# Kernel tuning notes

Measured on AMD Instinct MI355X. Metric: run time of the kernel, lower is better.

The kernel has to match this reference:

```python
import jax, jax.numpy as jnp
import numpy as np

B, N, D, C, K = 16, 1024, 64, 64, 20
EPS = 1e-3  # keras BatchNormalization default epsilon


def _bn(x, g, b, mu, v):
    return (x - mu) * jax.lax.rsqrt(v + EPS) * g + b


def setup_inputs() -> dict:
    key = jax.random.key(0)
    ks = jax.random.split(key, 6)
    return {
        "feats": jax.random.normal(ks[0], (B, N, D), dtype=jnp.float32),
        "adj": jax.random.uniform(ks[1], (B, N, N), dtype=jnp.float32),
        "w1": jax.random.normal(ks[2], (2 * D, C), dtype=jnp.float32) * 0.05,
        "b1": jax.random.normal(ks[3], (C,), dtype=jnp.float32) * 0.05,
        "g1": jnp.ones((C,), jnp.float32),
        "be1": jnp.zeros((C,), jnp.float32),
        "mu1": jnp.zeros((C,), jnp.float32),
        "v1": jnp.ones((C,), jnp.float32),
        "w2": jax.random.normal(ks[4], (C, C), dtype=jnp.float32) * 0.05,
        "b2": jax.random.normal(ks[5], (C,), dtype=jnp.float32) * 0.05,
        "g2": jnp.ones((C,), jnp.float32),
        "be2": jnp.zeros((C,), jnp.float32),
        "mu2": jnp.zeros((C,), jnp.float32),
        "v2": jnp.ones((C,), jnp.float32),
        "k": K,
    }


def reference(feats, adj, w1, b1, g1, be1, mu1, v1, w2, b2, g2, be2, mu2, v2, k):
    # weighted distance matrix from feature channel 0
    f0 = feats[:, :, 0]                                   # (B,N)
    fdiff = jnp.abs(f0[:, None, :] - f0[:, :, None])       # |f[j]-f[i]| at (b,i,j)
    a = adj * fdiff                                        # (B,N,N)
    # KNN: top_k of negated distance
    _, nn_idx = jax.lax.top_k(-a, k)                       # (B,N,k)
    # edge feature gather
    knn_fts = jax.vmap(lambda f, idx: f[idx])(feats, nn_idx)          # (B,N,k,D)
    center = jnp.broadcast_to(feats[:, :, None, :], knn_fts.shape)    # (B,N,k,D)
    edge = jnp.concatenate([center, knn_fts - center], axis=-1)       # (B,N,k,2D)
    # two fused 1x1 conv + BN + ReLU
    x = jax.nn.relu(_bn(jnp.einsum('bnkd,dc->bnkc', edge, w1) + b1, g1, be1, mu1, v1))
    x = jax.nn.relu(_bn(jnp.einsum('bnkc,ce->bnke', x, w2) + b2, g2, be2, mu2, v2))
    # mean over neighbors
    return jnp.mean(x, axis=2)                             # (B,N,C)
```

## Files before the change

kernel.cpp:

```cpp
#include <hip/hip_runtime.h>
#include <float.h>
#include <math.h>

#define NN 1024
#define DD 64
#define CC 64
#define KK 20
#define EPSL 1e-3f

typedef __attribute__((ext_vector_type(8))) short short8;
typedef __attribute__((ext_vector_type(4))) float f32x4;

__device__ __forceinline__ unsigned short f2bf(float f) {
    unsigned u = __float_as_uint(f);
    return (unsigned short)((u + 0x7fffu + ((u >> 16) & 1u)) >> 16);
}

__global__ __launch_bounds__(256) void k0_f0(const float* __restrict__ feats,
                                             float* __restrict__ f0c) {
    int u = blockIdx.x * 256 + threadIdx.x;
    f0c[u] = feats[(size_t)u * DD];
}

__global__ __launch_bounds__(256) void k2_topk_prep(
        const float* __restrict__ adj, const float* __restrict__ f0c,
        const float* __restrict__ w1, const float* __restrict__ w2,
        const float* __restrict__ b1, const float* __restrict__ g1,
        const float* __restrict__ be1, const float* __restrict__ mu1,
        const float* __restrict__ v1,
        unsigned short* __restrict__ b1t, unsigned short* __restrict__ w2t,
        float* __restrict__ bb, int* __restrict__ nnidx) {
    int t = blockIdx.x * 256 + threadIdx.x;
    if (t < 8192) {
        int n = t >> 6, k = t & 63;
        float val;
        if (n < 64) {
            float s = g1[n] * rsqrtf(v1[n] + EPSL);
            val = (w1[k * CC + n] - w1[(k + DD) * CC + n]) * s;
        } else {
            int c = n - 64;
            float s = g1[c] * rsqrtf(v1[c] + EPSL);
            val = w1[(k + DD) * CC + c] * s;
        }
        b1t[t] = f2bf(val);
    } else if (t < 12288) {
        int i = t - 8192;
        int n = i >> 6, k = i & 63;
        w2t[i] = f2bf(w2[k * CC + n]);
    } else if (t < 12352) {
        int c = t - 12288;
        float s = g1[c] * rsqrtf(v1[c] + EPSL);
        bb[c] = b1[c] * s + be1[c] - mu1[c] * s;
    }

    int lane = threadIdx.x & 63;
    int w    = threadIdx.x >> 6;
    int row  = blockIdx.x * 4 + w;
    int b    = row >> 10;
    __shared__ unsigned long long keybuf[4][64];
    const float4* arow = (const float4*)(adj + (size_t)row * NN);
    const float4* frow = (const float4*)(f0c + (size_t)b * NN);
    float f0i = f0c[row];
    unsigned vu[16];
#pragma unroll
    for (int tv = 0; tv < 4; ++tv) {
        float4 av = arow[64 * tv + lane];
        float4 fv = frow[64 * tv + lane];
        vu[tv * 4 + 0] = __float_as_uint(av.x * fabsf(fv.x - f0i));
        vu[tv * 4 + 1] = __float_as_uint(av.y * fabsf(fv.y - f0i));
        vu[tv * 4 + 2] = __float_as_uint(av.z * fabsf(fv.z - f0i));
        vu[tv * 4 + 3] = __float_as_uint(av.w * fabsf(fv.w - f0i));
    }
    unsigned x = vu[0];
#pragma unroll
    for (int tt = 1; tt < 16; ++tt) x = (vu[tt] < x) ? vu[tt] : x;
#pragma unroll
    for (int k = 2; k <= 64; k <<= 1) {
#pragma unroll
        for (int j = k >> 1; j > 0; j >>= 1) {
            unsigned o = __shfl_xor(x, j);
            bool keepmin = (((lane & j) == 0) == ((lane & k) == 0));
            unsigned mn = (o < x) ? o : x;
            unsigned mx = (o < x) ? x : o;
            x = keepmin ? mn : mx;
        }
    }
    unsigned T = __shfl(x, 19);
    int cnt = 0;
#pragma unroll
    for (int tt = 0; tt < 16; ++tt) cnt += (vu[tt] <= T) ? 1 : 0;
    int inc = cnt;
#pragma unroll
    for (int off = 1; off < 64; off <<= 1) {
        int o = __shfl_up(inc, off);
        if (lane >= off) inc += o;
    }
    int total = __shfl(inc, 63);
    int* outp = nnidx + (size_t)row * KK;

    if (total <= 64) {
        int pos = inc - cnt;
#pragma unroll
        for (int tt = 0; tt < 16; ++tt) {
            if (vu[tt] <= T) {
                int j = 256 * (tt >> 2) + 4 * lane + (tt & 3);
                keybuf[w][pos] = ((unsigned long long)vu[tt] << 32) | (unsigned)j;
                pos++;
            }
        }
        unsigned long long key = (lane < total) ? keybuf[w][lane] : ~0ull;
        unsigned y = (unsigned)(key >> 32);
#pragma unroll
        for (int k = 2; k <= 64; k <<= 1) {
#pragma unroll
            for (int j = k >> 1; j > 0; j >>= 1) {
                unsigned o = __shfl_xor(y, j);
                bool keepmin = (((lane & j) == 0) == ((lane & k) == 0));
                unsigned mn = (o < y) ? o : y;
                unsigned mx = (o < y) ? y : o;
                y = keepmin ? mn : mx;
            }
        }
        unsigned Tstar = __shfl(y, 19);
        bool fl = (lane < total) && ((unsigned)(key >> 32) <= Tstar);
        unsigned long long msk = __ballot(fl);
        int p = __popcll(msk & ((1ull << lane) - 1ull));
        if (fl && p < KK) outp[p] = (int)(unsigned)key;
    } else {
        for (int r = 0; r < KK; ++r) {
            unsigned bv = vu[0];
            int bt = 0;
#pragma unroll
            for (int tt = 1; tt < 16; ++tt) {
                if (vu[tt] < bv) { bv = vu[tt]; bt = tt; }
            }
            int bj = 256 * (bt >> 2) + 4 * lane + (bt & 3);
            unsigned wv = bv;
            int wi = bj;
#pragma unroll
            for (int m = 1; m < 64; m <<= 1) {
                unsigned ov = __shfl_xor(wv, m);
                int oi = __shfl_xor(wi, m);
                if (ov < wv || (ov == wv && oi < wi)) { wv = ov; wi = oi; }
            }
            if (lane == 0) outp[r] = wi;
            if (((wi >> 2) & 63) == lane) {
                int s = ((wi >> 8) << 2) | (wi & 3);
#pragma unroll
                for (int tt = 0; tt < 16; ++tt) {
                    if (tt == s) vu[tt] = 0xFFFFFFFFu;
                }
            }
        }
    }
}

__global__ __launch_bounds__(256) void k1_mfma(
        const float* __restrict__ feats, const unsigned short* __restrict__ b1t,
        const float* __restrict__ bb,
        unsigned short* __restrict__ cterm, unsigned short* __restrict__ nterm) {
    int lane = threadIdx.x & 63, w = threadIdx.x >> 6;
    int col = lane & 15, quad = lane >> 4;
    int m0 = blockIdx.x * 16;
    int nb = w * 32;

    short8 bfr[2][2];
#pragma unroll
    for (int nt = 0; nt < 2; ++nt)
#pragma unroll
        for (int ks = 0; ks < 2; ++ks)
            bfr[nt][ks] = *(const short8*)(b1t + (nb + nt * 16 + col) * 64 + ks * 32 + quad * 8);

    float bbv[2] = {0.f, 0.f};
    if (w < 2) {
        bbv[0] = bb[nb + col];
        bbv[1] = bb[nb + 16 + col];
    }

    f32x4 acc[2];
    acc[0] = (f32x4)(0.f);
    acc[1] = (f32x4)(0.f);

    const float* fr = feats + (size_t)(m0 + col) * DD;
#pragma unroll
    for (int ks = 0; ks < 2; ++ks) {
        float4 p0 = *(const float4*)(fr + ks * 32 + quad * 8);
        float4 p1 = *(const float4*)(fr + ks * 32 + quad * 8 + 4);
        float f[8] = {p0.x, p0.y, p0.z, p0.w, p1.x, p1.y, p1.z, p1.w};
        uint4 hp, lp;
        unsigned hw[4], lw[4];
#pragma unroll
        for (int d = 0; d < 4; ++d) {
            float a = f[2 * d], bq = f[2 * d + 1];
            unsigned ua = __float_as_uint(a), ub = __float_as_uint(bq);
            unsigned am = ua & 0xffff0000u, bm = ub & 0xffff0000u;
            float ra = a - __uint_as_float(am);
            float rb = bq - __uint_as_float(bm);
            hw[d] = bm | (ua >> 16);
            lw[d] = (__float_as_uint(rb) & 0xffff0000u) | (__float_as_uint(ra) >> 16);
        }
        hp.x = hw[0]; hp.y = hw[1]; hp.z = hw[2]; hp.w = hw[3];
        lp.x = lw[0]; lp.y = lw[1]; lp.z = lw[2]; lp.w = lw[3];
        short8 ah = __builtin_bit_cast(short8, hp);
        short8 al = __builtin_bit_cast(short8, lp);
#pragma unroll
        for (int nt = 0; nt < 2; ++nt) {
            acc[nt] = __builtin_amdgcn_mfma_f32_16x16x32_bf16(ah, bfr[nt][ks], acc[nt], 0, 0, 0);
            acc[nt] = __builtin_amdgcn_mfma_f32_16x16x32_bf16(al, bfr[nt][ks], acc[nt], 0, 0, 0);
        }
    }

#pragma unroll
    for (int nt = 0; nt < 2; ++nt) {
        int n = nb + nt * 16 + col;
#pragma unroll
        for (int r = 0; r < 4; ++r) {
            int m = m0 + quad * 4 + r;
            unsigned short v = f2bf(acc[nt][r] + bbv[nt]);
            if (w < 2) cterm[(size_t)m * CC + n] = v;
            else       nterm[(size_t)m * CC + (n - 64)] = v;
        }
    }
}

__global__ __launch_bounds__(256, 3) void k3_mfma(
        const unsigned short* __restrict__ cterm, const unsigned short* __restrict__ nterm,
        const int* __restrict__ nnidx, const unsigned short* __restrict__ w2t,
        const float* __restrict__ b2,
        const float* __restrict__ g2, const float* __restrict__ be2,
        const float* __restrict__ mu2, const float* __restrict__ v2,
        float* __restrict__ out) {
    int lane = threadIdx.x & 63, w = threadIdx.x >> 6;
    int col = lane & 15, quad = lane >> 4;
    int wid = blockIdx.x * 4 + w;
    int u0 = wid * 4;
    int b  = u0 >> 10;

    short8 bfr[4][2];
#pragma unroll
    for (int nt = 0; nt < 4; ++nt)
#pragma unroll
        for (int ks = 0; ks < 2; ++ks)
            bfr[nt][ks] = *(const short8*)(w2t + (nt * 16 + col) * 64 + ks * 32 + quad * 8);

    float s2v[4], sh2v[4];
#pragma unroll
    for (int nt = 0; nt < 4; ++nt) {
        int c = nt * 16 + col;
        float s2 = g2[c] * rsqrtf(v2[c] + EPSL);
        s2v[nt]  = s2;
        sh2v[nt] = (b2[c] - mu2[c]) * s2 + be2[c];
    }

    f32x4 acc[5][4];
#pragma unroll
    for (int mt = 0; mt < 5; ++mt)
#pragma unroll
        for (int nt = 0; nt < 4; ++nt) acc[mt][nt] = (f32x4)(0.f);

    const int* ibase = nnidx + (size_t)u0 * KK;
    int jrow[5];
#pragma unroll
    for (int mt = 0; mt < 5; ++mt) jrow[mt] = ibase[mt * 16 + col];

#pragma unroll
    for (int mt = 0; mt < 5; ++mt) {
        int row = mt * 16 + col;
        int g   = (row * 205) >> 12;
        const unsigned short* np = nterm + (size_t)(b * NN + jrow[mt]) * CC;
        const unsigned short* cp = cterm + (size_t)(u0 + g) * CC;
        short8 afr[2];
#pragma unroll
        for (int ks = 0; ks < 2; ++ks) {
            int ch = ks * 32 + quad * 8;
            uint4 cv = *(const uint4*)(cp + ch);
            uint4 nv = *(const uint4*)(np + ch);
            unsigned cw[4] = {cv.x, cv.y, cv.z, cv.w};
            unsigned nw[4] = {nv.x, nv.y, nv.z, nv.w};
            uint4 rp;
            unsigned rw[4];
#pragma unroll
            for (int d = 0; d < 4; ++d) {
                float cl  = __uint_as_float(cw[d] << 16);
                float chh = __uint_as_float(cw[d] & 0xffff0000u);
                float nl  = __uint_as_float(nw[d] << 16);
                float nhh = __uint_as_float(nw[d] & 0xffff0000u);
                float sl = fmaxf(cl + nl, 0.f);
                float sh = fmaxf(chh + nhh, 0.f);
                rw[d] = (__float_as_uint(sh) & 0xffff0000u) | (__float_as_uint(sl) >> 16);
            }
            rp.x = rw[0]; rp.y = rw[1]; rp.z = rw[2]; rp.w = rw[3];
            afr[ks] = __builtin_bit_cast(short8, rp);
        }
#pragma unroll
        for (int ks = 0; ks < 2; ++ks)
#pragma unroll
            for (int nt = 0; nt < 4; ++nt)
                acc[mt][nt] = __builtin_amdgcn_mfma_f32_16x16x32_bf16(afr[ks], bfr[nt][ks], acc[mt][nt], 0, 0, 0);
    }

    float us0[4] = {0,0,0,0}, us1[4] = {0,0,0,0}, us2[4] = {0,0,0,0}, us3[4] = {0,0,0,0};
#pragma unroll
    for (int mt = 0; mt < 5; ++mt)
#pragma unroll
        for (int nt = 0; nt < 4; ++nt) {
            float qs = 0.f;
#pragma unroll
            for (int r = 0; r < 4; ++r)
                qs += fmaxf(acc[mt][nt][r] * s2v[nt] + sh2v[nt], 0.f);
            if (mt == 0) us0[nt] += qs;
            else if (mt == 4) us3[nt] += qs;
            else if (mt == 1) { float t = (quad >= 1) ? qs : 0.f; us1[nt] += t; us0[nt] += qs - t; }
            else if (mt == 2) { float t = (quad >= 2) ? qs : 0.f; us2[nt] += t; us1[nt] += qs - t; }
            else              { float t = (quad >= 3) ? qs : 0.f; us3[nt] += t; us2[nt] += qs - t; }
        }
#pragma unroll
    for (int nt = 0; nt < 4; ++nt) {
        us0[nt] += __shfl_xor(us0[nt], 16); us0[nt] += __shfl_xor(us0[nt], 32);
        us1[nt] += __shfl_xor(us1[nt], 16); us1[nt] += __shfl_xor(us1[nt], 32);
        us2[nt] += __shfl_xor(us2[nt], 16); us2[nt] += __shfl_xor(us2[nt], 32);
        us3[nt] += __shfl_xor(us3[nt], 16); us3[nt] += __shfl_xor(us3[nt], 32);
    }
#pragma unroll
    for (int nt = 0; nt < 4; ++nt) {
        float v = (quad == 0) ? us0[nt] : (quad == 1) ? us1[nt] : (quad == 2) ? us2[nt] : us3[nt];
        out[(size_t)(u0 + quad) * CC + nt * 16 + col] = v * 0.05f;
    }
}

extern "C" void kernel_launch(void* const* d_in, const int* in_sizes, int n_in,
                              void* d_out, int out_size, void* d_ws, size_t ws_size,
                              hipStream_t stream) {
    const float* feats = (const float*)d_in[0];
    const float* adj   = (const float*)d_in[1];
    const float* w1    = (const float*)d_in[2];
    const float* b1    = (const float*)d_in[3];
    const float* g1    = (const float*)d_in[4];
    const float* be1   = (const float*)d_in[5];
    const float* mu1   = (const float*)d_in[6];
    const float* v1    = (const float*)d_in[7];
    const float* w2    = (const float*)d_in[8];
    const float* b2    = (const float*)d_in[9];
    const float* g2    = (const float*)d_in[10];
    const float* be2   = (const float*)d_in[11];
    const float* mu2   = (const float*)d_in[12];
    const float* v2    = (const float*)d_in[13];
    float* out = (float*)d_out;

    char* ws = (char*)d_ws;
    unsigned short* cterm = (unsigned short*)(ws);
    unsigned short* nterm = (unsigned short*)(ws + 2u * 1024 * 1024);
    int*            nnidx = (int*)  (ws + 4u * 1024 * 1024);
    unsigned short* b1t   = (unsigned short*)(ws + 6u * 1024 * 1024);
    unsigned short* w2t   = (unsigned short*)(ws + 6u * 1024 * 1024 + 16u * 1024);
    float*          bb    = (float*)(ws + 6u * 1024 * 1024 + 24u * 1024);
    float*          f0c   = (float*)(ws + 6u * 1024 * 1024 + 32u * 1024);

    k0_f0<<<64, 256, 0, stream>>>(feats, f0c);
    k2_topk_prep<<<4096, 256, 0, stream>>>(adj, f0c, w1, w2, b1,
                                           g1, be1, mu1, v1,
                                           b1t, w2t, bb, nnidx);
    k1_mfma<<<1024, 256, 0, stream>>>(feats, b1t, bb, cterm, nterm);
    k3_mfma<<<1024, 256, 0, stream>>>(cterm, nterm, nnidx, w2t, b2,
                                      g2, be2, mu2, v2, out);
}
```

Measured before the change: 147.4 us.

## Fold f0 extraction and weight prep into first MFMA kernel, drop a launch

Removes the standalone f0 extraction kernel and the weight-prep code that ran inside the top-k kernel. The first MFMA kernel now builds its BN-folded bf16 W1 fragments directly from w1 in registers, writes f0c as a side output and converts w2, and it is launched before the top-k kernel. The adjacency read in top-k switches to nontemporal loads. This saves one launch and the b1t/bb round trip through memory, but every block now recomputes the W1 folding with strided global reads.

```diff
diff --git a/kernel.cpp b/kernel.cpp
--- a/kernel.cpp
+++ b/kernel.cpp
@@ -16,55 +16,118 @@
     return (unsigned short)((u + 0x7fffu + ((u >> 16) & 1u)) >> 16);
 }
 
-__global__ __launch_bounds__(256) void k0_f0(const float* __restrict__ feats,
-                                             float* __restrict__ f0c) {
-    int u = blockIdx.x * 256 + threadIdx.x;
-    f0c[u] = feats[(size_t)u * DD];
-}
-
-__global__ __launch_bounds__(256) void k2_topk_prep(
-        const float* __restrict__ adj, const float* __restrict__ f0c,
-        const float* __restrict__ w1, const float* __restrict__ w2,
+__global__ __launch_bounds__(256) void k1_mfma(
+        const float* __restrict__ feats, const float* __restrict__ w1,
         const float* __restrict__ b1, const float* __restrict__ g1,
         const float* __restrict__ be1, const float* __restrict__ mu1,
-        const float* __restrict__ v1,
-        unsigned short* __restrict__ b1t, unsigned short* __restrict__ w2t,
-        float* __restrict__ bb, int* __restrict__ nnidx) {
+        const float* __restrict__ v1, const float* __restrict__ w2,
+        unsigned short* __restrict__ cterm, unsigned short* __restrict__ nterm,
+        float* __restrict__ f0c, unsigned short* __restrict__ w2t) {
     int t = blockIdx.x * 256 + threadIdx.x;
-    if (t < 8192) {
+    if (t < 4096) {
         int n = t >> 6, k = t & 63;
-        float val;
-        if (n < 64) {
-            float s = g1[n] * rsqrtf(v1[n] + EPSL);
-            val = (w1[k * CC + n] - w1[(k + DD) * CC + n]) * s;
-        } else {
-            int c = n - 64;
-            float s = g1[c] * rsqrtf(v1[c] + EPSL);
-            val = w1[(k + DD) * CC + c] * s;
-        }
-        b1t[t] = f2bf(val);
-    } else if (t < 12288) {
-        int i = t - 8192;
-        int n = i >> 6, k = i & 63;
-        w2t[i] = f2bf(w2[k * CC + n]);
-    } else if (t < 12352) {
-        int c = t - 12288;
-        float s = g1[c] * rsqrtf(v1[c] + EPSL);
-        bb[c] = b1[c] * s + be1[c] - mu1[c] * s;
-    }
-
+        w2t[t] = f2bf(w2[k * CC + n]);
+    }
+
+    int lane = threadIdx.x & 63, w = threadIdx.x >> 6;
+    int col = lane & 15, quad = lane >> 4;
+    int m0 = blockIdx.x * 16;
+    int nb = w * 32;
+
+    int c0 = nb + col;
+    int cc0 = (w < 2) ? c0 : c0 - 64;
+    int cc1 = cc0 + 16;
+    float s1a = g1[cc0] * rsqrtf(v1[cc0] + EPSL);
+    float s1b = g1[cc1] * rsqrtf(v1[cc1] + EPSL);
+    float bbv[2] = {0.f, 0.f};
+    if (w < 2) {
+        bbv[0] = b1[cc0] * s1a + be1[cc0] - mu1[cc0] * s1a;
+        bbv[1] = b1[cc1] * s1b + be1[cc1] - mu1[cc1] * s1b;
+    }
+
+    short8 bfr[2][2];
+#pragma unroll
+    for (int nt = 0; nt < 2; ++nt) {
+        int cc = nt ? cc1 : cc0;
+        float ss = nt ? s1b : s1a;
+#pragma unroll
+        for (int ks = 0; ks < 2; ++ks) {
+#pragma unroll
+            for (int i = 0; i < 8; ++i) {
+                int d = ks * 32 + quad * 8 + i;
+                float wv;
+                if (w < 2) wv = (w1[d * CC + cc] - w1[(d + DD) * CC + cc]) * ss;
+                else       wv = w1[(d + DD) * CC + cc] * ss;
+                bfr[nt][ks][i] = (short)f2bf(wv);
+            }
+        }
+    }
+
+    f32x4 acc[2];
+    acc[0] = (f32x4)(0.f);
+    acc[1] = (f32x4)(0.f);
+
+    const float* fr = feats + (size_t)(m0 + col) * DD;
+    float f0save = 0.f;
+#pragma unroll
+    for (int ks = 0; ks < 2; ++ks) {
+        float4 p0 = *(const float4*)(fr + ks * 32 + quad * 8);
+        float4 p1 = *(const float4*)(fr + ks * 32 + quad * 8 + 4);
+        if (ks == 0) f0save = p0.x;
+        float f[8] = {p0.x, p0.y, p0.z, p0.w, p1.x, p1.y, p1.z, p1.w};
+        uint4 hp, lp;
+        unsigned hw[4], lw[4];
+#pragma unroll
+        for (int d = 0; d < 4; ++d) {
+            float a = f[2 * d], bq = f[2 * d + 1];
+            unsigned ua = __float_as_uint(a), ub = __float_as_uint(bq);
+            unsigned am = ua & 0xffff0000u, bm = ub & 0xffff0000u;
+            float ra = a - __uint_as_float(am);
+            float rb = bq - __uint_as_float(bm);
+            hw[d] = bm | (ua >> 16);
+            lw[d] = (__float_as_uint(rb) & 0xffff0000u) | (__float_as_uint(ra) >> 16);
+        }
+        hp.x = hw[0]; hp.y = hw[1]; hp.z = hw[2]; hp.w = hw[3];
+        lp.x = lw[0]; lp.y = lw[1]; lp.z = lw[2]; lp.w = lw[3];
+        short8 ah = __builtin_bit_cast(short8, hp);
+        short8 al = __builtin_bit_cast(short8, lp);
+#pragma unroll
+        for (int nt = 0; nt < 2; ++nt) {
+            acc[nt] = __builtin_amdgcn_mfma_f32_16x16x32_bf16(ah, bfr[nt][ks], acc[nt], 0, 0, 0);
+            acc[nt] = __builtin_amdgcn_mfma_f32_16x16x32_bf16(al, bfr[nt][ks], acc[nt], 0, 0, 0);
+        }
+    }
+
+    if (w == 0 && quad == 0) f0c[m0 + col] = f0save;
+
+#pragma unroll
+    for (int nt = 0; nt < 2; ++nt) {
+        int n = nb + nt * 16 + col;
+#pragma unroll
+        for (int r = 0; r < 4; ++r) {
+            int m = m0 + quad * 4 + r;
+            unsigned short v = f2bf(acc[nt][r] + bbv[nt]);
+            if (w < 2) cterm[(size_t)m * CC + n] = v;
+            else       nterm[(size_t)m * CC + (n - 64)] = v;
+        }
+    }
+}
+
+__global__ __launch_bounds__(256) void k2_topk(const float* __restrict__ adj,
+                                               const float* __restrict__ f0c,
+                                               int* __restrict__ nnidx) {
+    __shared__ unsigned long long keybuf[4][64];
     int lane = threadIdx.x & 63;
     int w    = threadIdx.x >> 6;
     int row  = blockIdx.x * 4 + w;
     int b    = row >> 10;
-    __shared__ unsigned long long keybuf[4][64];
-    const float4* arow = (const float4*)(adj + (size_t)row * NN);
+    const f32x4* arow = (const f32x4*)(adj + (size_t)row * NN);
     const float4* frow = (const float4*)(f0c + (size_t)b * NN);
     float f0i = f0c[row];
     unsigned vu[16];
 #pragma unroll
     for (int tv = 0; tv < 4; ++tv) {
-        float4 av = arow[64 * tv + lane];
+        f32x4 av = __builtin_nontemporal_load(&arow[64 * tv + lane]);
         float4 fv = frow[64 * tv + lane];
         vu[tv * 4 + 0] = __float_as_uint(av.x * fabsf(fv.x - f0i));
         vu[tv * 4 + 1] = __float_as_uint(av.y * fabsf(fv.y - f0i));
@@ -151,74 +214,6 @@
                     if (tt == s) vu[tt] = 0xFFFFFFFFu;
                 }
             }
-        }
-    }
-}
-
-__global__ __launch_bounds__(256) void k1_mfma(
-        const float* __restrict__ feats, const unsigned short* __restrict__ b1t,
-        const float* __restrict__ bb,
-        unsigned short* __restrict__ cterm, unsigned short* __restrict__ nterm) {
-    int lane = threadIdx.x & 63, w = threadIdx.x >> 6;
-    int col = lane & 15, quad = lane >> 4;
-    int m0 = blockIdx.x * 16;
-    int nb = w * 32;
-
-    short8 bfr[2][2];
-#pragma unroll
-    for (int nt = 0; nt < 2; ++nt)
-#pragma unroll
-        for (int ks = 0; ks < 2; ++ks)
-            bfr[nt][ks] = *(const short8*)(b1t + (nb + nt * 16 + col) * 64 + ks * 32 + quad * 8);
-
-    float bbv[2] = {0.f, 0.f};
-    if (w < 2) {
-        bbv[0] = bb[nb + col];
-        bbv[1] = bb[nb + 16 + col];
-    }
-
-    f32x4 acc[2];
-    acc[0] = (f32x4)(0.f);
-    acc[1] = (f32x4)(0.f);
-
-    const float* fr = feats + (size_t)(m0 + col) * DD;
-#pragma unroll
-    for (int ks = 0; ks < 2; ++ks) {
-        float4 p0 = *(const float4*)(fr + ks * 32 + quad * 8);
-        float4 p1 = *(const float4*)(fr + ks * 32 + quad * 8 + 4);
-        float f[8] = {p0.x, p0.y, p0.z, p0.w, p1.x, p1.y, p1.z, p1.w};
-        uint4 hp, lp;
-        unsigned hw[4], lw[4];
-#pragma unroll
-        for (int d = 0; d < 4; ++d) {
-            float a = f[2 * d], bq = f[2 * d + 1];
-            unsigned ua = __float_as_uint(a), ub = __float_as_uint(bq);
-            unsigned am = ua & 0xffff0000u, bm = ub & 0xffff0000u;
-            float ra = a - __uint_as_float(am);
-            float rb = bq - __uint_as_float(bm);
-            hw[d] = bm | (ua >> 16);
-            lw[d] = (__float_as_uint(rb) & 0xffff0000u) | (__float_as_uint(ra) >> 16);
-        }
-        hp.x = hw[0]; hp.y = hw[1]; hp.z = hw[2]; hp.w = hw[3];
-        lp.x = lw[0]; lp.y = lw[1]; lp.z = lw[2]; lp.w = lw[3];
-        short8 ah = __builtin_bit_cast(short8, hp);
-        short8 al = __builtin_bit_cast(short8, lp);
-#pragma unroll
-        for (int nt = 0; nt < 2; ++nt) {
-            acc[nt] = __builtin_amdgcn_mfma_f32_16x16x32_bf16(ah, bfr[nt][ks], acc[nt], 0, 0, 0);
-            acc[nt] = __builtin_amdgcn_mfma_f32_16x16x32_bf16(al, bfr[nt][ks], acc[nt], 0, 0, 0);
-        }
-    }
-
-#pragma unroll
-    for (int nt = 0; nt < 2; ++nt) {
-        int n = nb + nt * 16 + col;
-#pragma unroll
-        for (int r = 0; r < 4; ++r) {
-            int m = m0 + quad * 4 + r;
-            unsigned short v = f2bf(acc[nt][r] + bbv[nt]);
-            if (w < 2) cterm[(size_t)m * CC + n] = v;
-            else       nterm[(size_t)m * CC + (n - 64)] = v;
         }
     }
 }
@@ -351,16 +346,12 @@
     unsigned short* cterm = (unsigned short*)(ws);
     unsigned short* nterm = (unsigned short*)(ws + 2u * 1024 * 1024);
     int*            nnidx = (int*)  (ws + 4u * 1024 * 1024);
-    unsigned short* b1t   = (unsigned short*)(ws + 6u * 1024 * 1024);
-    unsigned short* w2t   = (unsigned short*)(ws + 6u * 1024 * 1024 + 16u * 1024);
-    float*          bb    = (float*)(ws + 6u * 1024 * 1024 + 24u * 1024);
-    float*          f0c   = (float*)(ws + 6u * 1024 * 1024 + 32u * 1024);
-
-    k0_f0<<<64, 256, 0, stream>>>(feats, f0c);
-    k2_topk_prep<<<4096, 256, 0, stream>>>(adj, f0c, w1, w2, b1,
-                                           g1, be1, mu1, v1,
-                                           b1t, w2t, bb, nnidx);
-    k1_mfma<<<1024, 256, 0, stream>>>(feats, b1t, bb, cterm, nterm);
+    unsigned short* w2t   = (unsigned short*)(ws + 6u * 1024 * 1024);
+    float*          f0c   = (float*)(ws + 6u * 1024 * 1024 + 16u * 1024);
+
+    k1_mfma<<<1024, 256, 0, stream>>>(feats, w1, b1, g1, be1, mu1, v1, w2,
+                                      cterm, nterm, f0c, w2t);
+    k2_topk<<<4096, 256, 0, stream>>>(adj, f0c, nnidx);
     k3_mfma<<<1024, 256, 0, stream>>>(cterm, nterm, nnidx, w2t, b2,
                                       g2, be2, mu2, v2, out);
 }
```

Result: slower. 155.8 us (+5.7%).
